# Kernel tuning notes

Hardware: AMD Instinct MI355X
Metric: run time of the kernel (lower is better)

Reference implementation:

```python
import jax, jax.numpy as jnp
import numpy as np

CHEB_K = 3
EMBED_DIM = 16
DIM_IN = 64
DIM_OUT = 64


def setup_inputs() -> dict:
    key = jax.random.key(0)
    k1, k2, k3, k4, k5 = jax.random.split(key, 5)
    B, N, C, D = 32, 2048, DIM_IN, EMBED_DIM
    x = jax.random.normal(k1, (B, N, C), dtype=jnp.float32)
    node_embeddings = jax.random.normal(k2, (N, D), dtype=jnp.float32)
    # scale lap so Chebyshev recursion (2*lap @ T - T_prev) stays well-conditioned
    lap = jax.random.normal(k3, (N, N), dtype=jnp.float32) / jnp.sqrt(jnp.float32(N))
    # add_apt=True -> weights_pool has cheb_k+1 supports
    weights_pool = jax.random.normal(k4, (D, CHEB_K + 1, C, DIM_OUT), dtype=jnp.float32) * 0.05
    bias_pool = jax.random.normal(k5, (D, DIM_OUT), dtype=jnp.float32) * 0.05
    return {"x": x, "node_embeddings": node_embeddings, "lap": lap,
            "weights_pool": weights_pool, "bias_pool": bias_pool}


def reference(x, node_embeddings, lap, weights_pool, bias_pool):
    N = node_embeddings.shape[0]
    # Chebyshev support stack: [I, lap, T_k = 2*lap@T_{k-1} - T_{k-2}, ...]
    support_set = [jnp.eye(N, dtype=x.dtype), lap]
    for _ in range(2, CHEB_K):
        support_set.append(2.0 * lap @ support_set[-1] - support_set[-2])
    # adaptive support from node embeddings (add_apt=True)
    apt = jax.nn.softmax(jax.nn.relu(node_embeddings @ node_embeddings.T), axis=1)
    support_set.append(apt)
    supports = jnp.stack(support_set, axis=0)                       # (K, N, N)
    # per-node dynamic weights / bias generated from node embeddings
    weights = jnp.einsum('nd,dkio->nkio', node_embeddings, weights_pool)  # (N,K,I,O)
    bias = node_embeddings @ bias_pool                              # (N, O)
    # support-weighted feature aggregation
    x_g = jnp.einsum('knm,bmc->bknc', supports, x)                  # (B,K,N,C)
    x_g = jnp.transpose(x_g, (0, 2, 1, 3))                          # (B,N,K,C)
    # per-node batched matmul + bias
    out = jnp.einsum('bnki,nkio->bno', x_g, weights) + bias         # (B,N,O)
    return out
```

## Files before the change

kernel.cpp:

```cpp
#include <hip/hip_runtime.h>

#define NN 2048
#define BB 32
#define CC 64
#define DD 16

typedef unsigned short u16;
typedef __attribute__((ext_vector_type(8))) short bf8_t;
typedef __attribute__((ext_vector_type(4))) float f4_t;

__device__ __forceinline__ u16 f2bf(float f) {
  unsigned u = __float_as_uint(f);
  return (u16)((u + 0x7fffu + ((u >> 16) & 1u)) >> 16);
}
__device__ __forceinline__ float bf2f(u16 u) {
  return __uint_as_float(((unsigned)u) << 16);
}
__device__ __forceinline__ void gload_lds16(const u16* g, u16* l) {
  __builtin_amdgcn_global_load_lds((const __attribute__((address_space(1))) unsigned*)g,
                                   (__attribute__((address_space(3))) unsigned*)l, 16, 0, 0);
}

__global__ __launch_bounds__(256) void cvt_bf16(const float* __restrict__ in,
                                                u16* __restrict__ outp) {
  const size_t i = ((size_t)blockIdx.x * 256 + threadIdx.x) * 8;
  const float4 v0 = *(const float4*)(in + i);
  const float4 v1 = *(const float4*)(in + i + 4);
  ushort4 a, b;
  a.x = f2bf(v0.x); a.y = f2bf(v0.y); a.z = f2bf(v0.z); a.w = f2bf(v0.w);
  b.x = f2bf(v1.x); b.y = f2bf(v1.y); b.z = f2bf(v1.z); b.w = f2bf(v1.w);
  *(ushort4*)(outp + i) = a;
  *(ushort4*)(outp + i + 4) = b;
}

__global__ __launch_bounds__(256) void apt_kernel(const float* __restrict__ E,
                                                  u16* __restrict__ apt) {
  __shared__ __align__(16) float s[NN];
  __shared__ float red[8];
  const int n = blockIdx.x;
  const int t = threadIdx.x;
  const float4* en4 = (const float4*)(E + (size_t)n * DD);
  const float4 e0 = en4[0], e1 = en4[1], e2 = en4[2], e3 = en4[3];
  float lmax = 0.f;
  for (int j = t; j < NN; j += 256) {
    const float4* ej = (const float4*)(E + (size_t)j * DD);
    const float4 a = ej[0], b = ej[1], c = ej[2], d = ej[3];
    float dot = e0.x*a.x + e0.y*a.y + e0.z*a.z + e0.w*a.w;
    dot += e1.x*b.x + e1.y*b.y + e1.z*b.z + e1.w*b.w;
    dot += e2.x*c.x + e2.y*c.y + e2.z*c.z + e2.w*c.w;
    dot += e3.x*d.x + e3.y*d.y + e3.z*d.z + e3.w*d.w;
    dot = fmaxf(dot, 0.f);
    s[j] = dot;
    lmax = fmaxf(lmax, dot);
  }
  #pragma unroll
  for (int off = 32; off > 0; off >>= 1) lmax = fmaxf(lmax, __shfl_down(lmax, off));
  if ((t & 63) == 0) red[t >> 6] = lmax;
  __syncthreads();
  const float gmax = fmaxf(fmaxf(red[0], red[1]), fmaxf(red[2], red[3]));
  float lsum = 0.f;
  for (int j = t; j < NN; j += 256) {
    const float e = __expf(s[j] - gmax);
    s[j] = e;
    lsum += e;
  }
  #pragma unroll
  for (int off = 32; off > 0; off >>= 1) lsum += __shfl_down(lsum, off);
  if ((t & 63) == 0) red[4 + (t >> 6)] = lsum;
  __syncthreads();
  const float inv = 1.f / (red[4] + red[5] + red[6] + red[7]);
  u16* aprow = apt + (size_t)n * NN;
  for (int j = t; j < NN; j += 256) aprow[j] = f2bf(s[j] * inv);
}

__global__ __launch_bounds__(256) void tr_f32_bf16(const float* __restrict__ in,
                                                   u16* __restrict__ outT) {
  __shared__ u16 T[64][65];
  const int b = blockIdx.y, m0 = blockIdx.x * 64, t = threadIdx.x;
  #pragma unroll
  for (int ii = 0; ii < 16; ++ii) {
    const int idx = t + 256 * ii;
    const int r = idx >> 6, c = idx & 63;
    T[c][r] = f2bf(in[((size_t)b * NN + m0 + r) * CC + c]);
  }
  __syncthreads();
  #pragma unroll
  for (int ii = 0; ii < 16; ++ii) {
    const int idx = t + 256 * ii;
    const int c = idx >> 6, r = idx & 63;
    outT[((size_t)b * CC + c) * NN + m0 + r] = T[c][r];
  }
}

__global__ __launch_bounds__(256) void tr_bf16(const u16* __restrict__ in,
                                               u16* __restrict__ outT) {
  __shared__ u16 T[64][65];
  const int b = blockIdx.y, m0 = blockIdx.x * 64, t = threadIdx.x;
  #pragma unroll
  for (int ii = 0; ii < 16; ++ii) {
    const int idx = t + 256 * ii;
    const int r = idx >> 6, c = idx & 63;
    T[c][r] = in[((size_t)b * NN + m0 + r) * CC + c];
  }
  __syncthreads();
  #pragma unroll
  for (int ii = 0; ii < 16; ++ii) {
    const int idx = t + 256 * ii;
    const int c = idx >> 6, r = idx & 63;
    outT[((size_t)b * CC + c) * NN + m0 + r] = T[c][r];
  }
}

__global__ __launch_bounds__(256) void mfma_gemm(
    const u16* __restrict__ A0, const u16* __restrict__ X0, const float* __restrict__ add0,
    float alpha0, float beta0, u16* __restrict__ Y0,
    const u16* __restrict__ A1, const u16* __restrict__ X1, const float* __restrict__ add1,
    float alpha1, float beta1, u16* __restrict__ Y1) {
  __shared__ __align__(16) u16 Alds[128 * 32];
  __shared__ __align__(16) u16 Blds[128 * 32];
  const int z = blockIdx.z;
  const u16* Ap = z ? A1 : A0;
  const u16* Xp = z ? X1 : X0;
  const float* add = z ? add1 : add0;
  const float alpha = z ? alpha1 : alpha0;
  const float beta = z ? beta1 : beta0;
  u16* Y = z ? Y1 : Y0;

  const int t = threadIdx.x;
  const int n0 = blockIdx.x * 128;
  const int c0 = blockIdx.y * 128;

  const int l = t & 63;
  const int w = t >> 6;
  const int lr = l & 15;
  const int lg = l >> 4;
  const int wr = (w >> 1) * 64, wc = (w & 1) * 64;

  int aoff[4], boff[4];
  #pragma unroll
  for (int f = 0; f < 4; ++f) {
    const int r = wr + f * 16 + lr;
    aoff[f] = r * 64 + ((lg ^ ((r >> 1) & 3)) * 16);
    const int c = wc + f * 16 + lr;
    boff[f] = c * 64 + ((lg ^ ((c >> 1) & 3)) * 16);
  }

  f4_t acc[4][4];
  const f4_t zf = {0.f, 0.f, 0.f, 0.f};
  #pragma unroll
  for (int i = 0; i < 4; ++i)
    #pragma unroll
    for (int j = 0; j < 4; ++j) acc[i][j] = zf;

  auto stage = [&](int kt) {
    #pragma unroll
    for (int i = 0; i < 2; ++i) {
      const int q = i * 256 + t;
      const int r = q >> 2, ch = q & 3;
      const int cg = ch ^ ((r >> 1) & 3);
      gload_lds16(Ap + (size_t)(n0 + r) * NN + kt + cg * 8, &Alds[q * 8]);
      gload_lds16(Xp + (size_t)(c0 + r) * NN + kt + cg * 8, &Blds[q * 8]);
    }
  };

  stage(0);
  for (int kt = 0; kt < NN; kt += 32) {
    __syncthreads();
    bf8_t a[4], b[4];
    #pragma unroll
    for (int f = 0; f < 4; ++f) a[f] = *(const bf8_t*)((const char*)Alds + aoff[f]);
    #pragma unroll
    for (int f = 0; f < 4; ++f) b[f] = *(const bf8_t*)((const char*)Blds + boff[f]);
    __syncthreads();
    if (kt + 32 < NN) stage(kt + 32);
    #pragma unroll
    for (int i = 0; i < 4; ++i)
      #pragma unroll
      for (int j = 0; j < 4; ++j)
        acc[i][j] = __builtin_amdgcn_mfma_f32_16x16x32_bf16(a[i], b[j], acc[i][j], 0, 0, 0);
  }

  #pragma unroll
  for (int i = 0; i < 4; ++i) {
    #pragma unroll
    for (int j = 0; j < 4; ++j) {
      const int col = c0 + wc + j * 16 + lr;
      const int bb = col >> 6, cc = col & 63;
      #pragma unroll
      for (int v = 0; v < 4; ++v) {
        const int row = n0 + wr + i * 16 + lg * 4 + v;
        const size_t o = ((size_t)bb * NN + row) * CC + cc;
        float val = alpha * acc[i][j][v];
        if (add) val = fmaf(beta, add[o], val);
        Y[o] = f2bf(val);
      }
    }
  }
}

__global__ __launch_bounds__(256) void out_kernel(const float* __restrict__ x,
                                                  const u16* __restrict__ y1,
                                                  const u16* __restrict__ y2,
                                                  const u16* __restrict__ y3,
                                                  const float* __restrict__ E,
                                                  const float* __restrict__ Wp,
                                                  const float* __restrict__ bp,
                                                  float* __restrict__ out) {
  __shared__ __align__(16) u16 Wl[2][16384];
  __shared__ __align__(16) float xgs[2][4][32][66];
  __shared__ float bias[2][64];
  __shared__ float en[2][16];
  const int n0 = blockIdx.x * 2;
  const int t = threadIdx.x;
  if (t < 32) en[t >> 4][t & 15] = E[(size_t)(n0 + (t >> 4)) * DD + (t & 15)];
  __syncthreads();
  for (int idx = t; idx < 16384; idx += 256) {
    float a0 = 0.f, a1 = 0.f;
    #pragma unroll
    for (int d = 0; d < 16; ++d) {
      const float wv = Wp[(size_t)d * 16384 + idx];
      a0 = fmaf(en[0][d], wv, a0);
      a1 = fmaf(en[1][d], wv, a1);
    }
    Wl[0][idx] = f2bf(a0);
    Wl[1][idx] = f2bf(a1);
  }
  if (t < 128) {
    const int nl = t >> 6, o = t & 63;
    float a = 0.f;
    #pragma unroll
    for (int d = 0; d < 16; ++d) a = fmaf(en[nl][d], bp[d * 64 + o], a);
    bias[nl][o] = a;
  }
  #pragma unroll 4
  for (int m = 0; m < 64; ++m) {
    const int idx = t + 256 * m;
    const int nl = idx >> 13, k = (idx >> 11) & 3, b = (idx >> 6) & 31, i = idx & 63;
    const size_t src = ((size_t)b * NN + n0 + nl) * CC + i;
    float v;
    if (k == 0) v = x[src];
    else if (k == 1) v = bf2f(y1[src]);
    else if (k == 2) v = bf2f(y2[src]);
    else v = bf2f(y3[src]);
    xgs[nl][k][b][i] = v;
  }
  __syncthreads();
  const int nl = t >> 7, tt = t & 127;
  const int ob = tt & 15;
  const int bq = tt >> 4;
  float acc[4][4];
  #pragma unroll
  for (int i = 0; i < 4; ++i)
    #pragma unroll
    for (int j = 0; j < 4; ++j) acc[i][j] = 0.f;
  #pragma unroll
  for (int k = 0; k < 4; ++k) {
    #pragma unroll 8
    for (int i = 0; i < 64; ++i) {
      const ushort4 wu = *(const ushort4*)&Wl[nl][k * 4096 + i * 64 + ob * 4];
      const float w0 = bf2f(wu.x), w1 = bf2f(wu.y), w2 = bf2f(wu.z), w3 = bf2f(wu.w);
      #pragma unroll
      for (int bb = 0; bb < 4; ++bb) {
        const float xa = xgs[nl][k][bq * 4 + bb][i];
        acc[bb][0] = fmaf(xa, w0, acc[bb][0]);
        acc[bb][1] = fmaf(xa, w1, acc[bb][1]);
        acc[bb][2] = fmaf(xa, w2, acc[bb][2]);
        acc[bb][3] = fmaf(xa, w3, acc[bb][3]);
      }
    }
  }
  #pragma unroll
  for (int bb = 0; bb < 4; ++bb) {
    float4 v;
    v.x = acc[bb][0] + bias[nl][ob * 4 + 0];
    v.y = acc[bb][1] + bias[nl][ob * 4 + 1];
    v.z = acc[bb][2] + bias[nl][ob * 4 + 2];
    v.w = acc[bb][3] + bias[nl][ob * 4 + 3];
    *(float4*)(out + ((size_t)(bq * 4 + bb) * NN + n0 + nl) * CC + ob * 4) = v;
  }
}

extern "C" void kernel_launch(void* const* d_in, const int* in_sizes, int n_in,
                              void* d_out, int out_size, void* d_ws, size_t ws_size,
                              hipStream_t stream) {
  const float* x   = (const float*)d_in[0];
  const float* E   = (const float*)d_in[1];
  const float* lap = (const float*)d_in[2];
  const float* Wp  = (const float*)d_in[3];
  const float* bp  = (const float*)d_in[4];
  float* out = (float*)d_out;

  char* ws = (char*)d_ws;
  const size_t SEG = (size_t)NN * NN * sizeof(u16);
  u16* lapB = (u16*)(ws);
  u16* aptB = (u16*)(ws + SEG);
  u16* xT   = (u16*)(ws + 2 * SEG);
  u16* y1n  = (u16*)(ws + 3 * SEG);
  u16* y1T  = (u16*)(ws + 4 * SEG);
  u16* y2n  = (u16*)(ws + 5 * SEG);
  u16* y3n  = (u16*)(ws + 6 * SEG);

  cvt_bf16<<<2048, 256, 0, stream>>>(lap, lapB);
  apt_kernel<<<NN, 256, 0, stream>>>(E, aptB);
  tr_f32_bf16<<<dim3(32, 32), 256, 0, stream>>>(x, xT);
  mfma_gemm<<<dim3(16, 16, 1), 256, 0, stream>>>(
      lapB, xT, nullptr, 1.f, 0.f, y1n,
      nullptr, nullptr, nullptr, 0.f, 0.f, nullptr);
  tr_bf16<<<dim3(32, 32), 256, 0, stream>>>(y1n, y1T);
  mfma_gemm<<<dim3(16, 16, 2), 256, 0, stream>>>(
      lapB, y1T, x, 2.f, -1.f, y2n,
      aptB, xT, nullptr, 1.f, 0.f, y3n);
  out_kernel<<<NN / 2, 256, 0, stream>>>(x, y1n, y2n, y3n, E, Wp, bp, out);
  (void)in_sizes; (void)n_in; (void)out_size; (void)ws_size;
}
```

Before: 405.4 us.

## Split per-node weight generation into separate kernel and use MFMA for final contraction

New measurement: 351.2 us. -13.4%, faster.

```diff
diff --git a/kernel.cpp b/kernel.cpp
--- a/kernel.cpp
+++ b/kernel.cpp
@@ -73,15 +73,18 @@
   for (int j = t; j < NN; j += 256) aprow[j] = f2bf(s[j] * inv);
 }
 
-__global__ __launch_bounds__(256) void tr_f32_bf16(const float* __restrict__ in,
-                                                   u16* __restrict__ outT) {
+__global__ __launch_bounds__(256) void trx_kernel(const float* __restrict__ in,
+                                                  u16* __restrict__ outT,
+                                                  u16* __restrict__ outB) {
   __shared__ u16 T[64][65];
   const int b = blockIdx.y, m0 = blockIdx.x * 64, t = threadIdx.x;
   #pragma unroll
   for (int ii = 0; ii < 16; ++ii) {
     const int idx = t + 256 * ii;
     const int r = idx >> 6, c = idx & 63;
-    T[c][r] = f2bf(in[((size_t)b * NN + m0 + r) * CC + c]);
+    const u16 v = f2bf(in[((size_t)b * NN + m0 + r) * CC + c]);
+    T[c][r] = v;
+    outB[((size_t)b * NN + m0 + r) * CC + c] = v;
   }
   __syncthreads();
   #pragma unroll
@@ -198,85 +201,105 @@
   }
 }
 
-__global__ __launch_bounds__(256) void out_kernel(const float* __restrict__ x,
-                                                  const u16* __restrict__ y1,
-                                                  const u16* __restrict__ y2,
-                                                  const u16* __restrict__ y3,
-                                                  const float* __restrict__ E,
-                                                  const float* __restrict__ Wp,
-                                                  const float* __restrict__ bp,
-                                                  float* __restrict__ out) {
-  __shared__ __align__(16) u16 Wl[2][16384];
-  __shared__ __align__(16) float xgs[2][4][32][66];
-  __shared__ float bias[2][64];
-  __shared__ float en[2][16];
-  const int n0 = blockIdx.x * 2;
+__global__ __launch_bounds__(256) void wgen_kernel(const float* __restrict__ E,
+                                                   const float* __restrict__ Wp,
+                                                   u16* __restrict__ Wt, int n0base) {
+  __shared__ u16 wp[16][32][64];
+  __shared__ float es[8][16];
   const int t = threadIdx.x;
-  if (t < 32) en[t >> 4][t & 15] = E[(size_t)(n0 + (t >> 4)) * DD + (t & 15)];
-  __syncthreads();
-  for (int idx = t; idx < 16384; idx += 256) {
-    float a0 = 0.f, a1 = 0.f;
-    #pragma unroll
-    for (int d = 0; d < 16; ++d) {
-      const float wv = Wp[(size_t)d * 16384 + idx];
-      a0 = fmaf(en[0][d], wv, a0);
-      a1 = fmaf(en[1][d], wv, a1);
+  const int ng = n0base + blockIdx.x * 8;
+  const int nl = blockIdx.x * 8;
+  if (t < 128) es[t >> 4][t & 15] = E[(size_t)(ng + (t >> 4)) * DD + (t & 15)];
+  const int ki = t & 31, og = t >> 5;
+  for (int kc = 0; kc < 8; ++kc) {
+    __syncthreads();
+    #pragma unroll 8
+    for (int jj = 0; jj < 32; ++jj) {
+      const int idx4 = jj * 256 + t;
+      const int e = idx4 * 4;
+      const int d = e >> 11, rem = e & 2047, kk = rem >> 6, o = rem & 63;
+      const float4 v = *(const float4*)(Wp + (size_t)d * 16384 + (size_t)(kc * 32 + kk) * 64 + o);
+      ushort4 u;
+      u.x = f2bf(v.x); u.y = f2bf(v.y); u.z = f2bf(v.z); u.w = f2bf(v.w);
+      *(ushort4*)&wp[d][kk][o ^ ((kk & 7) << 3)] = u;
     }
-    Wl[0][idx] = f2bf(a0);
-    Wl[1][idx] = f2bf(a1);
-  }
-  if (t < 128) {
-    const int nl = t >> 6, o = t & 63;
-    float a = 0.f;
-    #pragma unroll
-    for (int d = 0; d < 16; ++d) a = fmaf(en[nl][d], bp[d * 64 + o], a);
-    bias[nl][o] = a;
-  }
-  #pragma unroll 4
-  for (int m = 0; m < 64; ++m) {
-    const int idx = t + 256 * m;
-    const int nl = idx >> 13, k = (idx >> 11) & 3, b = (idx >> 6) & 31, i = idx & 63;
-    const size_t src = ((size_t)b * NN + n0 + nl) * CC + i;
-    float v;
-    if (k == 0) v = x[src];
-    else if (k == 1) v = bf2f(y1[src]);
-    else if (k == 2) v = bf2f(y2[src]);
-    else v = bf2f(y3[src]);
-    xgs[nl][k][b][i] = v;
-  }
-  __syncthreads();
-  const int nl = t >> 7, tt = t & 127;
-  const int ob = tt & 15;
-  const int bq = tt >> 4;
-  float acc[4][4];
-  #pragma unroll
-  for (int i = 0; i < 4; ++i)
-    #pragma unroll
-    for (int j = 0; j < 4; ++j) acc[i][j] = 0.f;
-  #pragma unroll
-  for (int k = 0; k < 4; ++k) {
-    #pragma unroll 8
-    for (int i = 0; i < 64; ++i) {
-      const ushort4 wu = *(const ushort4*)&Wl[nl][k * 4096 + i * 64 + ob * 4];
-      const float w0 = bf2f(wu.x), w1 = bf2f(wu.y), w2 = bf2f(wu.z), w3 = bf2f(wu.w);
+    __syncthreads();
+    for (int oo = 0; oo < 8; ++oo) {
+      const int o = og * 8 + oo;
+      float wv[16];
       #pragma unroll
-      for (int bb = 0; bb < 4; ++bb) {
-        const float xa = xgs[nl][k][bq * 4 + bb][i];
-        acc[bb][0] = fmaf(xa, w0, acc[bb][0]);
-        acc[bb][1] = fmaf(xa, w1, acc[bb][1]);
-        acc[bb][2] = fmaf(xa, w2, acc[bb][2]);
-        acc[bb][3] = fmaf(xa, w3, acc[bb][3]);
+      for (int d = 0; d < 16; ++d) wv[d] = bf2f(wp[d][ki][o ^ ((ki & 7) << 3)]);
+      #pragma unroll
+      for (int nn = 0; nn < 8; ++nn) {
+        float a = 0.f;
+        #pragma unroll
+        for (int d = 0; d < 16; ++d) a = fmaf(es[nn][d], wv[d], a);
+        Wt[(size_t)(nl + nn) * 16384 + o * 256 + kc * 32 + ki] = f2bf(a);
       }
     }
   }
-  #pragma unroll
-  for (int bb = 0; bb < 4; ++bb) {
-    float4 v;
-    v.x = acc[bb][0] + bias[nl][ob * 4 + 0];
-    v.y = acc[bb][1] + bias[nl][ob * 4 + 1];
-    v.z = acc[bb][2] + bias[nl][ob * 4 + 2];
-    v.w = acc[bb][3] + bias[nl][ob * 4 + 3];
-    *(float4*)(out + ((size_t)(bq * 4 + bb) * NN + n0 + nl) * CC + ob * 4) = v;
+}
+
+__global__ __launch_bounds__(256) void final_kernel(const u16* __restrict__ xB,
+                                                    const u16* __restrict__ y1,
+                                                    const u16* __restrict__ y2,
+                                                    const u16* __restrict__ y3,
+                                                    const u16* __restrict__ Wt,
+                                                    const float* __restrict__ E,
+                                                    const float* __restrict__ bp,
+                                                    float* __restrict__ out, int nbase) {
+  __shared__ __align__(16) u16 Wl[64 * 256];
+  __shared__ __align__(16) u16 xga[32 * 256];
+  __shared__ float bias[64];
+  const int n = nbase + blockIdx.x;
+  const int t = threadIdx.x;
+  const u16* wsrc = Wt + (size_t)(n - nbase) * 16384;
+  #pragma unroll
+  for (int j = 0; j < 8; ++j) {
+    const int q = j * 256 + t;
+    const int r = q >> 5, ch = q & 31;
+    const int cg = ch ^ (r & 7);
+    gload_lds16(wsrc + r * 256 + cg * 8, &Wl[q * 8]);
+  }
+  #pragma unroll
+  for (int j = 0; j < 4; ++j) {
+    const int q = j * 256 + t;
+    const int r = q >> 5, ch = q & 31;
+    const int cg = ch ^ (r & 7);
+    const int kbuf = cg >> 3, i = (cg & 7) * 8;
+    const u16* src = (kbuf == 0) ? xB : (kbuf == 1) ? y1 : (kbuf == 2) ? y2 : y3;
+    gload_lds16(src + ((size_t)r * NN + n) * CC + i, &xga[q * 8]);
+  }
+  if (t < 64) {
+    float a = 0.f;
+    #pragma unroll
+    for (int d = 0; d < 16; ++d) a = fmaf(E[(size_t)n * DD + d], bp[d * 64 + t], a);
+    bias[t] = a;
+  }
+  __syncthreads();
+
+  const int l = t & 63, w = t >> 6;
+  const int lr = l & 15, lg = l >> 4;
+  const int mt = w >> 1;
+  const int nb = (w & 1) * 2;
+  const int arow = mt * 16 + lr;
+  const int brow0 = nb * 16 + lr, brow1 = (nb + 1) * 16 + lr;
+  f4_t acc0 = {0.f, 0.f, 0.f, 0.f}, acc1 = {0.f, 0.f, 0.f, 0.f};
+  #pragma unroll
+  for (int kt = 0; kt < 8; ++kt) {
+    const int c = kt * 4 + lg;
+    const bf8_t a  = *(const bf8_t*)&xga[arow * 256 + (c ^ (arow & 7)) * 8];
+    const bf8_t b0 = *(const bf8_t*)&Wl[brow0 * 256 + (c ^ (brow0 & 7)) * 8];
+    const bf8_t b1 = *(const bf8_t*)&Wl[brow1 * 256 + (c ^ (brow1 & 7)) * 8];
+    acc0 = __builtin_amdgcn_mfma_f32_16x16x32_bf16(a, b0, acc0, 0, 0, 0);
+    acc1 = __builtin_amdgcn_mfma_f32_16x16x32_bf16(a, b1, acc1, 0, 0, 0);
+  }
+  const int o0 = nb * 16 + lr, o1 = (nb + 1) * 16 + lr;
+  #pragma unroll
+  for (int v = 0; v < 4; ++v) {
+    const int b = mt * 16 + lg * 4 + v;
+    out[((size_t)b * NN + n) * CC + o0] = acc0[v] + bias[o0];
+    out[((size_t)b * NN + n) * CC + o1] = acc1[v] + bias[o1];
   }
 }
 
@@ -295,14 +318,16 @@
   u16* lapB = (u16*)(ws);
   u16* aptB = (u16*)(ws + SEG);
   u16* xT   = (u16*)(ws + 2 * SEG);
-  u16* y1n  = (u16*)(ws + 3 * SEG);
-  u16* y1T  = (u16*)(ws + 4 * SEG);
+  u16* y1T  = (u16*)(ws + 3 * SEG);
+  u16* y1n  = (u16*)(ws + 4 * SEG);
   u16* y2n  = (u16*)(ws + 5 * SEG);
   u16* y3n  = (u16*)(ws + 6 * SEG);
+  u16* xB   = (u16*)(ws + 7 * SEG);
+  u16* Wth  = (u16*)(ws);
 
   cvt_bf16<<<2048, 256, 0, stream>>>(lap, lapB);
   apt_kernel<<<NN, 256, 0, stream>>>(E, aptB);
-  tr_f32_bf16<<<dim3(32, 32), 256, 0, stream>>>(x, xT);
+  trx_kernel<<<dim3(32, 32), 256, 0, stream>>>(x, xT, xB);
   mfma_gemm<<<dim3(16, 16, 1), 256, 0, stream>>>(
       lapB, xT, nullptr, 1.f, 0.f, y1n,
       nullptr, nullptr, nullptr, 0.f, 0.f, nullptr);
@@ -310,6 +335,9 @@
   mfma_gemm<<<dim3(16, 16, 2), 256, 0, stream>>>(
       lapB, y1T, x, 2.f, -1.f, y2n,
       aptB, xT, nullptr, 1.f, 0.f, y3n);
-  out_kernel<<<NN / 2, 256, 0, stream>>>(x, y1n, y2n, y3n, E, Wp, bp, out);
+  wgen_kernel<<<128, 256, 0, stream>>>(E, Wp, Wth, 0);
+  final_kernel<<<1024, 256, 0, stream>>>(xB, y1n, y2n, y3n, Wth, E, bp, out, 0);
+  wgen_kernel<<<128, 256, 0, stream>>>(E, Wp, Wth, 1024);
+  final_kernel<<<1024, 256, 0, stream>>>(xB, y1n, y2n, y3n, Wth, E, bp, out, 1024);
   (void)in_sizes; (void)n_in; (void)out_size; (void)ws_size;
 }
```
